# Kernel optimization log

Hardware: AMD Instinct MI355X
Metric: run time of the kernel (lower is better)

Reference implementation:

```python
import jax, jax.numpy as jnp
import numpy as np

B, S, H = 2, 1024, 2048
NH, HD = 16, 128
L = 4  # num_prev_layers == attention_window


def _rope(x):
    # x: [..., S, D]; standard rotate-half RoPE, base 10000
    d = x.shape[-1]
    s = x.shape[-2]
    inv_freq = 1.0 / (10000.0 ** (jnp.arange(0, d, 2, dtype=jnp.float32) / d))
    freqs = jnp.outer(jnp.arange(s, dtype=jnp.float32), inv_freq)  # [S, d/2]
    cos, sin = jnp.cos(freqs), jnp.sin(freqs)
    x1, x2 = jnp.split(x, 2, axis=-1)
    return jnp.concatenate([x1 * cos - x2 * sin, x2 * cos + x1 * sin], axis=-1)


def setup_inputs() -> dict:
    key = jax.random.key(0)
    ks = jax.random.split(key, 8)
    std = 0.02
    return {
        "hidden_states": jax.random.normal(ks[0], (B, S, H), jnp.float32),
        "prev_hidden_states": jax.random.normal(ks[1], (L, B, S, H), jnp.float32),
        "Wq": jax.random.normal(ks[2], (H, NH * HD), jnp.float32) * std,
        "bq": jnp.zeros((NH * HD,), jnp.float32),
        "Wk": jax.random.normal(ks[3], (H, NH * HD), jnp.float32) * std,
        "bk": jnp.zeros((NH * HD,), jnp.float32),
        "Wv": jax.random.normal(ks[4], (H, NH * HD), jnp.float32) * std,
        "bv": jnp.zeros((NH * HD,), jnp.float32),
        "Wo": jax.random.normal(ks[5], (NH * HD, H), jnp.float32) * std,
        "bo": jnp.zeros((H,), jnp.float32),
        "Wg": jax.random.normal(ks[6], (H, L), jnp.float32) * std,
    }


def reference(hidden_states, prev_hidden_states, Wq, bq, Wk, bk, Wv, bv, Wo, bo, Wg):
    b, s, _ = hidden_states.shape
    # queries from current layer: [b, nh, s, hd], RoPE applied
    q = (hidden_states @ Wq + bq).reshape(b, s, NH, HD).transpose(0, 2, 1, 3)
    q = _rope(q)
    # keys/values from each prev layer: [L, b, nh, s, hd]
    k = (prev_hidden_states @ Wk + bk).reshape(L, b, s, NH, HD).transpose(0, 1, 3, 2, 4)
    k = _rope(k)
    v = (prev_hidden_states @ Wv + bv).reshape(L, b, s, NH, HD).transpose(0, 1, 3, 2, 4)
    # per-prev-layer attention (no mask)
    scores = jnp.einsum('bhqd,lbhkd->lbhqk', q, k) / jnp.sqrt(jnp.float32(HD))
    attn = jax.nn.softmax(scores, axis=-1)
    lo = jnp.einsum('lbhqk,lbhkd->lbhqd', attn, v)
    lo = lo.transpose(0, 1, 3, 2, 4).reshape(L, b, s, NH * HD)  # merge heads
    # softmax gate over pooled queries -> combine layer outputs
    layer_w = jax.nn.softmax(jnp.mean(hidden_states, axis=1) @ Wg, axis=-1)  # [b, L]
    out = jnp.einsum('lbsh,bl->bsh', lo, layer_w)
    return out @ Wo + bo
```

## Files before the change

kernel.cpp:

```cpp
#include <hip/hip_runtime.h>
#include <hip/hip_bf16.h>
#include <math.h>


typedef __bf16 bf16;
typedef __bf16 bf16x4v __attribute__((ext_vector_type(4)));
typedef __bf16 bf16x8 __attribute__((ext_vector_type(8)));
typedef float f32x4 __attribute__((ext_vector_type(4)));

#define DEV static __device__ __forceinline__

DEV void gload_lds16(const void* g, void* s) {
  __builtin_amdgcn_global_load_lds(
      (const __attribute__((address_space(1))) void*)g,
      (__attribute__((address_space(3))) void*)s, 16, 0, 0);
}

DEV f32x4 mfma16(bf16x8 a, bf16x8 b, f32x4 c) {
  return __builtin_amdgcn_mfma_f32_16x16x32_bf16(a, b, c, 0, 0, 0);
}

__global__ __launch_bounds__(256) void cvt_kernel(const float* __restrict__ in,
                                                  bf16* __restrict__ out, int n4) {
  int i = blockIdx.x * 256 + threadIdx.x;
  if (i >= n4) return;
  const float4 v = ((const float4*)in)[i];
  bf16x4v o;
  o.x = (bf16)v.x; o.y = (bf16)v.y; o.z = (bf16)v.z; o.w = (bf16)v.w;
  ((bf16x4v*)out)[i] = o;
}

__global__ __launch_bounds__(256) void twt_kernel(const float* __restrict__ W,
                                                  bf16* __restrict__ Wt) {
  __shared__ float tile[64][65];
  const int t = threadIdx.x;
  const int n0 = blockIdx.x * 64, k0 = blockIdx.y * 64;
#pragma unroll
  for (int ph = 0; ph < 16; ++ph) {
    int idx = ph * 256 + t, r = idx >> 6, c = idx & 63;
    tile[r][c] = W[(size_t)(k0 + r) * 2048 + n0 + c];
  }
  __syncthreads();
#pragma unroll
  for (int ph = 0; ph < 16; ++ph) {
    int idx = ph * 256 + t, r = idx >> 6, c = idx & 63;
    Wt[(size_t)(n0 + r) * 2048 + k0 + c] = (bf16)tile[c][r];
  }
}

__global__ __launch_bounds__(64) void rope_table_kernel(float* __restrict__ cosT,
                                                        float* __restrict__ sinT) {
  int s = blockIdx.x, j = threadIdx.x;
  float inv = powf(10000.0f, -(float)j * (1.0f / 64.0f));
  float a = (float)s * inv;
  cosT[s * 64 + j] = cosf(a);
  sinT[s * 64 + j] = sinf(a);
}

__global__ __launch_bounds__(256) void rope_kernel(const bf16* __restrict__ raw,
                                                   const float* __restrict__ cosT,
                                                   const float* __restrict__ sinT,
                                                   bf16* __restrict__ outp) {
  int rid = blockIdx.x * 16 + (threadIdx.x >> 4);
  int j = threadIdx.x & 15;
  int s = rid & 1023;
  const bf16* src = raw + (size_t)rid * 128 + 4 * j;
  bf16* dst = outp + (size_t)rid * 128 + 4 * j;
  bf16x4v x1 = *(const bf16x4v*)src;
  bf16x4v x2 = *(const bf16x4v*)(src + 64);
  f32x4 c = *(const f32x4*)(cosT + s * 64 + 4 * j);
  f32x4 sn = *(const f32x4*)(sinT + s * 64 + 4 * j);
  bf16x4v o1, o2;
#pragma unroll
  for (int k = 0; k < 4; ++k) {
    float a = (float)x1[k], b2 = (float)x2[k];
    o1[k] = (bf16)(a * c[k] - b2 * sn[k]);
    o2[k] = (bf16)(b2 * c[k] + a * sn[k]);
  }
  *(bf16x4v*)dst = o1;
  *(bf16x4v*)(dst + 64) = o2;
}

__global__ __launch_bounds__(256) void mean_part_kernel(const float* __restrict__ hs,
                                                        float* __restrict__ part) {
  int bc = blockIdx.x;
  int b = bc >> 3, c0 = (bc & 7) * 256;
  int ss = blockIdx.y;
  int col = c0 + threadIdx.x;
  float s = 0.f;
  for (int r = 0; r < 128; ++r)
    s += hs[((size_t)b * 1024 + ss * 128 + r) * 2048 + col];
  part[(size_t)ss * 4096 + b * 2048 + col] = s;
}

__global__ __launch_bounds__(256) void mean_fin_kernel(const float* __restrict__ part,
                                                       float* __restrict__ meanb) {
  int c = blockIdx.x * 256 + threadIdx.x;
  float s = 0.f;
#pragma unroll
  for (int j = 0; j < 8; ++j) s += part[(size_t)j * 4096 + c];
  meanb[c] = s * (1.0f / 1024.0f);
}

__global__ __launch_bounds__(256) void gate_kernel(const float* __restrict__ meanb,
                                                   const float* __restrict__ Wg,
                                                   float* __restrict__ lwout) {
  __shared__ float red[8][256];
  int t = threadIdx.x;
  float p[8];
#pragma unroll
  for (int j = 0; j < 8; ++j) p[j] = 0.f;
  for (int hh = t; hh < 2048; hh += 256) {
    float m0 = meanb[hh], m1 = meanb[2048 + hh];
#pragma unroll
    for (int ll = 0; ll < 4; ++ll) {
      float g = Wg[hh * 4 + ll];
      p[ll] += m0 * g;
      p[4 + ll] += m1 * g;
    }
  }
#pragma unroll
  for (int j = 0; j < 8; ++j) red[j][t] = p[j];
  __syncthreads();
  for (int s2 = 128; s2 > 0; s2 >>= 1) {
    if (t < s2) {
#pragma unroll
      for (int j = 0; j < 8; ++j) red[j][t] += red[j][t + s2];
    }
    __syncthreads();
  }
  if (t == 0) {
#pragma unroll
    for (int bb = 0; bb < 2; ++bb) {
      float v0 = red[bb * 4 + 0][0], v1 = red[bb * 4 + 1][0];
      float v2 = red[bb * 4 + 2][0], v3 = red[bb * 4 + 3][0];
      float mx = fmaxf(fmaxf(v0, v1), fmaxf(v2, v3));
      float e0 = __expf(v0 - mx), e1 = __expf(v1 - mx);
      float e2 = __expf(v2 - mx), e3 = __expf(v3 - mx);
      float inv = 1.0f / (e0 + e1 + e2 + e3);
      lwout[bb * 4 + 0] = e0 * inv;
      lwout[bb * 4 + 1] = e1 * inv;
      lwout[bb * 4 + 2] = e2 * inv;
      lwout[bb * 4 + 3] = e3 * inv;
    }
  }
}

template <int OUTMODE>
__global__ __launch_bounds__(256) void gemm_kernel(const bf16* __restrict__ A,
                                                   const bf16* __restrict__ Bt,
                                                   const float* __restrict__ bias,
                                                   void* __restrict__ Cout,
                                                   int M, int N, int K) {
  __shared__ __attribute__((aligned(16))) bf16 As[2][128 * 64];
  __shared__ __attribute__((aligned(16))) bf16 Bs[2][128 * 64];
  const int t = threadIdx.x;
  const int w = t >> 6, l = t & 63;
  const int lo = l & 15, hi = l >> 4;
  const int wr = w >> 1, wc = w & 1;

  const int nwg = gridDim.x * gridDim.y;
  int flat = blockIdx.y * gridDim.x + blockIdx.x;
  int swz = (flat & 7) * (nwg >> 3) + (flat >> 3);
  const int bx = swz % gridDim.x, by = swz / gridDim.x;

  f32x4 acc[4][4];
#pragma unroll
  for (int m = 0; m < 4; ++m)
#pragma unroll
    for (int n = 0; n < 4; ++n)
#pragma unroll
      for (int q = 0; q < 4; ++q) acc[m][n][q] = 0.f;

  int srow[4], scl[4];
#pragma unroll
  for (int p = 0; p < 4; ++p) {
    int id = p * 256 + t;
    int r = id >> 3, cph = id & 7;
    srow[p] = r;
    scl[p] = cph ^ (r & 7);
  }

  const bf16* Ab = A + (size_t)by * 128 * K;
  const bf16* Bb = Bt + (size_t)bx * 128 * K;

  auto stage = [&](int bi, int kt) {
#pragma unroll
    for (int p = 0; p < 4; ++p)
      gload_lds16(Ab + (size_t)srow[p] * K + kt + scl[p] * 8,
                  &As[bi][(p * 256 + w * 64) * 8]);
#pragma unroll
    for (int p = 0; p < 4; ++p)
      gload_lds16(Bb + (size_t)srow[p] * K + kt + scl[p] * 8,
                  &Bs[bi][(p * 256 + w * 64) * 8]);
  };

  stage(0, 0);
  int cur = 0;
  for (int kt = 0; kt < K; kt += 64) {
    if (kt + 64 < K) {
      stage(cur ^ 1, kt + 64);
      asm volatile("s_waitcnt vmcnt(8)" ::: "memory");
    } else {
      asm volatile("s_waitcnt vmcnt(0)" ::: "memory");
    }
    __builtin_amdgcn_s_barrier();
    __builtin_amdgcn_sched_barrier(0);
    __builtin_amdgcn_s_setprio(1);
#pragma unroll
    for (int ks = 0; ks < 2; ++ks) {
      bf16x8 af[4], bfr[4];
#pragma unroll
      for (int m = 0; m < 4; ++m) {
        int row = wr * 64 + m * 16 + lo;
        int ch = (ks * 4 + hi) ^ (row & 7);
        af[m] = *(const bf16x8*)&As[cur][row * 64 + ch * 8];
      }
#pragma unroll
      for (int n = 0; n < 4; ++n) {
        int row = wc * 64 + n * 16 + lo;
        int ch = (ks * 4 + hi) ^ (row & 7);
        bfr[n] = *(const bf16x8*)&Bs[cur][row * 64 + ch * 8];
      }
#pragma unroll
      for (int m = 0; m < 4; ++m)
#pragma unroll
        for (int n = 0; n < 4; ++n)
          acc[m][n] = mfma16(af[m], bfr[n], acc[m][n]);
    }
    __builtin_amdgcn_s_setprio(0);
    __builtin_amdgcn_s_barrier();
    cur ^= 1;
  }

#pragma unroll
  for (int n = 0; n < 4; ++n) {
    int col = bx * 128 + wc * 64 + n * 16 + lo;
    float bb = bias[col];
#pragma unroll
    for (int m = 0; m < 4; ++m) {
#pragma unroll
      for (int i = 0; i < 4; ++i) {
        size_t row = (size_t)by * 128 + wr * 64 + m * 16 + hi * 4 + i;
        float v = acc[m][n][i] + bb;
        if (OUTMODE == 1)
          ((float*)Cout)[row * N + col] = v;
        else if (OUTMODE == 0)
          ((bf16*)Cout)[row * N + col] = (bf16)v;
        else {
          size_t g = (row >> 10) * 16 + (col >> 7);
          ((bf16*)Cout)[(g * 1024 + (row & 1023)) * 128 + (col & 127)] = (bf16)v;
        }
      }
    }
  }
}

__global__ __launch_bounds__(512, 2) void gemm_kv_kernel(
    const bf16* __restrict__ prev, const bf16* __restrict__ WkT,
    const bf16* __restrict__ WvT, const float* __restrict__ bk,
    const float* __restrict__ bv, const float* __restrict__ cosT,
    const float* __restrict__ sinT, bf16* __restrict__ Kout,
    bf16* __restrict__ Vout) {
  __shared__ __attribute__((aligned(16))) bf16 As[2][16384];
  __shared__ __attribute__((aligned(16))) bf16 Bs[2][16384];
  const int t = threadIdx.x;
  const int w = t >> 6, l = t & 63;
  const int lo = l & 15, hi = l >> 4;
  const int wm = w >> 2, wn = w & 3;

  const int bid = blockIdx.x;
  const int grp = bid >> 8;
  const int sub = bid & 255;
  const int swz = (sub & 7) * 32 + (sub >> 3);
  const int mt = (grp == 0) ? (swz >> 3) : (swz & 7);
  const int nt = (grp == 0) ? (swz & 7) : (swz >> 3);
  const bf16* Ab = ((grp == 0) ? prev : WvT) + (size_t)mt * 256 * 2048;
  const bf16* Bb = ((grp == 0) ? WkT : prev) + (size_t)nt * 256 * 2048;

  const int r0 = t >> 2;
  const int c8 = ((t & 3) ^ ((r0 >> 1) & 3)) * 8;
  int r0B = r0;
  if (grp == 0) {
    int a = r0 >> 5, rr = r0 & 31;
    r0B = (a == 0) ? rr : (a == 1) ? rr + 64 : (a == 2) ? rr + 32 : rr + 96;
  }

  f32x4 acc[8][4];
#pragma unroll
  for (int m = 0; m < 8; ++m)
#pragma unroll
    for (int n = 0; n < 4; ++n)
#pragma unroll
      for (int q = 0; q < 4; ++q) acc[m][n][q] = 0.f;

  auto gA = [&](int bi, int kh, int p, int koff) {
    gload_lds16(Ab + (size_t)(p * 128 + r0) * 2048 + koff + kh * 32 + c8,
                &As[bi][kh * 8192 + p * 4096 + w * 512]);
  };
  auto gB = [&](int bi, int kh, int p, int koff) {
    gload_lds16(Bb + (size_t)(p * 128 + r0B) * 2048 + koff + kh * 32 + c8,
                &Bs[bi][kh * 8192 + p * 4096 + w * 512]);
  };

  gA(0, 0, 0, 0); gA(0, 0, 1, 0);
  gB(0, 0, 0, 0); gB(0, 0, 1, 0);
  gA(0, 1, 0, 0); gA(0, 1, 1, 0);
  gB(0, 1, 0, 0); gB(0, 1, 1, 0);
  asm volatile("s_waitcnt vmcnt(4)" ::: "memory");
  __builtin_amdgcn_s_barrier();

  int cur = 0;
  for (int kt = 0; kt < 32; ++kt) {
    const int nxt = cur ^ 1;
    const int koff = (kt + 1) * 64;
    const bool pf = kt < 31;
    bf16x8 af[8], bfr[2];

#pragma unroll
    for (int m = 0; m < 8; ++m) {
      int row = wm * 128 + m * 16 + lo;
      int slot = hi ^ ((row >> 1) & 3);
      af[m] = *(const bf16x8*)&As[cur][row * 32 + slot * 8];
    }
#pragma unroll
    for (int n = 0; n < 2; ++n) {
      int row = wn * 64 + n * 16 + lo;
      int slot = hi ^ ((row >> 1) & 3);
      bfr[n] = *(const bf16x8*)&Bs[cur][row * 32 + slot * 8];
    }
    if (pf) { gA(nxt, 0, 0, koff); gA(nxt, 0, 1, koff); }
    __builtin_amdgcn_s_barrier();
    __builtin_amdgcn_s_setprio(1);
#pragma unroll
    for (int m = 0; m < 8; ++m) {
      acc[m][0] = mfma16(af[m], bfr[0], acc[m][0]);
      acc[m][1] = mfma16(af[m], bfr[1], acc[m][1]);
    }
    __builtin_amdgcn_s_setprio(0);
    __builtin_amdgcn_s_barrier();

#pragma unroll
    for (int n = 0; n < 2; ++n) {
      int row = wn * 64 + (n + 2) * 16 + lo;
      int slot = hi ^ ((row >> 1) & 3);
      bfr[n] = *(const bf16x8*)&Bs[cur][row * 32 + slot * 8];
    }
    if (pf) {
      gB(nxt, 0, 0, koff); gB(nxt, 0, 1, koff);
      asm volatile("s_waitcnt vmcnt(4)" ::: "memory");
    } else {
      asm volatile("s_waitcnt vmcnt(0)" ::: "memory");
    }
    __builtin_amdgcn_s_barrier();
    __builtin_amdgcn_s_setprio(1);
#pragma unroll
    for (int m = 0; m < 8; ++m) {
      acc[m][2] = mfma16(af[m], bfr[0], acc[m][2]);
      acc[m][3] = mfma16(af[m], bfr[1], acc[m][3]);
    }
    __builtin_amdgcn_s_setprio(0);
    __builtin_amdgcn_s_barrier();

#pragma unroll
    for (int m = 0; m < 8; ++m) {
      int row = wm * 128 + m * 16 + lo;
      int slot = hi ^ ((row >> 1) & 3);
      af[m] = *(const bf16x8*)&As[cur][8192 + row * 32 + slot * 8];
    }
#pragma unroll
    for (int n = 0; n < 2; ++n) {
      int row = wn * 64 + n * 16 + lo;
      int slot = hi ^ ((row >> 1) & 3);
      bfr[n] = *(const bf16x8*)&Bs[cur][8192 + row * 32 + slot * 8];
    }
    if (pf) { gA(nxt, 1, 0, koff); gA(nxt, 1, 1, koff); }
    __builtin_amdgcn_s_barrier();
    __builtin_amdgcn_s_setprio(1);
#pragma unroll
    for (int m = 0; m < 8; ++m) {
      acc[m][0] = mfma16(af[m], bfr[0], acc[m][0]);
      acc[m][1] = mfma16(af[m], bfr[1], acc[m][1]);
    }
    __builtin_amdgcn_s_setprio(0);
    __builtin_amdgcn_s_barrier();

#pragma unroll
    for (int n = 0; n < 2; ++n) {
      int row = wn * 64 + (n + 2) * 16 + lo;
      int slot = hi ^ ((row >> 1) & 3);
      bfr[n] = *(const bf16x8*)&Bs[cur][8192 + row * 32 + slot * 8];
    }
    if (pf) {
      gB(nxt, 1, 0, koff); gB(nxt, 1, 1, koff);
      asm volatile("s_waitcnt vmcnt(4)" ::: "memory");
    } else {
      asm volatile("s_waitcnt vmcnt(0)" ::: "memory");
    }
    __builtin_amdgcn_s_barrier();
    __builtin_amdgcn_s_setprio(1);
#pragma unroll
    for (int m = 0; m < 8; ++m) {
      acc[m][2] = mfma16(af[m], bfr[0], acc[m][2]);
      acc[m][3] = mfma16(af[m], bfr[1], acc[m][3]);
    }
    __builtin_amdgcn_s_setprio(0);
    __builtin_amdgcn_s_barrier();

    cur = nxt;
  }

  if (grp == 0) {
    const int headg = nt * 2 + (wn >> 1);
    const int jbase = (wn & 1) * 32;
#pragma unroll
    for (int n = 0; n < 2; ++n) {
      int j = jbase + n * 16 + lo;
      float bb1 = bk[headg * 128 + j];
      float bb2 = bk[headg * 128 + j + 64];
#pragma unroll
      for (int m = 0; m < 8; ++m) {
#pragma unroll
        for (int i = 0; i < 4; ++i) {
          size_t srow = (size_t)mt * 256 + wm * 128 + m * 16 + hi * 4 + i;
          int s_idx = (int)(srow & 1023);
          size_t g = (srow >> 10) * 16 + headg;
          float x1 = acc[m][n][i] + bb1;
          float x2 = acc[m][n + 2][i] + bb2;
          float cc = cosT[s_idx * 64 + j];
          float ss = sinT[s_idx * 64 + j];
          bf16* dst = Kout + (g * 1024 + s_idx) * 128;
          dst[j] = (bf16)(x1 * cc - x2 * ss);
          dst[j + 64] = (bf16)(x2 * cc + x1 * ss);
        }
      }
    }
  } else {
#pragma unroll
    for (int m = 0; m < 8; ++m) {
#pragma unroll
      for (int i = 0; i < 4; ++i) {
        size_t row = (size_t)mt * 256 + wm * 128 + m * 16 + hi * 4 + i;
        float rb = bv[row];
#pragma unroll
        for (int n = 0; n < 4; ++n) {
          int col = nt * 256 + wn * 64 + n * 16 + lo;
          int pos64 = ((n >> 1) << 5) + ((lo >> 2) << 3) + ((n & 1) << 2) + (lo & 3);
          int colp = (col & ~63) | pos64;
          float v = acc[m][n][i] + rb;
          Vout[(size_t)(colp >> 10) * 2097152 + row * 1024 + (colp & 1023)] =
              (bf16)v;
        }
      }
    }
  }
}

__global__ __launch_bounds__(256, 2) void attn_kernel(const bf16* __restrict__ Q,
                                                      const bf16* __restrict__ Kb,
                                                      const bf16* __restrict__ Vt,
                                                      const float* __restrict__ lw,
                                                      bf16* __restrict__ Obuf) {
  __shared__ __attribute__((aligned(16))) bf16 Ks[2][64 * 128];
  __shared__ __attribute__((aligned(16))) bf16 Vs[2][128 * 64];
  const int t = threadIdx.x, w = t >> 6, l = t & 63;
  const int lo = l & 15, hi = l >> 4;
  const int bh = blockIdx.x;
  const int qt = blockIdx.y;
  const int li = blockIdx.z;
  const int b = bh >> 4, h = bh & 15;
  const float C2 = 0.08838834764831845f * 1.44269504f;
  const float M2 = 64.0f * C2;

  bf16x8 qf[2][4];
#pragma unroll
  for (int qs = 0; qs < 2; ++qs) {
    const bf16* qptr =
        Q + ((size_t)bh * 1024 + qt * 128 + w * 32 + qs * 16 + lo) * 128;
#pragma unroll
    for (int db = 0; db < 4; ++db)
      qf[qs][db] = *(const bf16x8*)(qptr + db * 32 + hi * 8);
  }

  int krow[4], kcl[4], vrow[4], vcl[4];
#pragma unroll
  for (int p = 0; p < 4; ++p) {
    int id = p * 256 + t;
    krow[p] = id >> 4;
    kcl[p] = (id & 15) ^ (krow[p] & 7);
    vrow[p] = id >> 3;
    vcl[p] = (id & 7) ^ (vrow[p] & 7);
  }

  const bf16* Kl = Kb + ((size_t)li * 32 + bh) * (size_t)131072;
  const bf16* Vl = Vt + ((size_t)li * 32 + bh) * (size_t)131072;

  float si0 = 0.f, si1 = 0.f;
  f32x4 oacc[2][8];
#pragma unroll
  for (int qs = 0; qs < 2; ++qs)
#pragma unroll
    for (int dc = 0; dc < 8; ++dc)
#pragma unroll
      for (int q = 0; q < 4; ++q) oacc[qs][dc][q] = 0.f;

  auto stage = [&](int bi, int kt2) {
    const bf16* Ksrc = Kl + (size_t)kt2 * 8192;
#pragma unroll
    for (int p = 0; p < 4; ++p)
      gload_lds16(Ksrc + (size_t)krow[p] * 128 + kcl[p] * 8,
                  &Ks[bi][(p * 256 + w * 64) * 8]);
#pragma unroll
    for (int p = 0; p < 4; ++p)
      gload_lds16(Vl + (size_t)vrow[p] * 1024 + kt2 * 64 + vcl[p] * 8,
                  &Vs[bi][(p * 256 + w * 64) * 8]);
  };

  auto softmax_step = [&](f32x4 (&sa)[4], float& si, bf16x8 (&pf2)[2]) {
    float rs = 0.f;
    bf16x4v pk[4];
#pragma unroll
    for (int kc = 0; kc < 4; ++kc) {
#pragma unroll
      for (int i = 0; i < 4; ++i) {
        float pf_ = __builtin_amdgcn_exp2f(fmaf(sa[kc][i], C2, -M2));
        rs += pf_;
        pk[kc][i] = (bf16)pf_;
      }
    }
    rs += __shfl_xor(rs, 16);
    rs += __shfl_xor(rs, 32);
    si += rs;
    pf2[0] = __builtin_shufflevector(pk[0], pk[1], 0, 1, 2, 3, 4, 5, 6, 7);
    pf2[1] = __builtin_shufflevector(pk[2], pk[3], 0, 1, 2, 3, 4, 5, 6, 7);
  };

  stage(0, 0);
  int cur = 0;
  for (int kt = 0; kt < 16; ++kt) {
    if (kt < 15) {
      stage(cur ^ 1, kt + 1);
      asm volatile("s_waitcnt vmcnt(8)" ::: "memory");
    } else {
      asm volatile("s_waitcnt vmcnt(0)" ::: "memory");
    }
    __builtin_amdgcn_s_barrier();
    __builtin_amdgcn_sched_barrier(0);

    f32x4 sa[2][4];
#pragma unroll
    for (int qs = 0; qs < 2; ++qs)
#pragma unroll
      for (int kc = 0; kc < 4; ++kc)
#pragma unroll
        for (int q = 0; q < 4; ++q) sa[qs][kc][q] = 0.f;
    __builtin_amdgcn_s_setprio(1);
#pragma unroll
    for (int kc = 0; kc < 4; ++kc) {
      int row = kc * 16 + lo;
#pragma unroll
      for (int db = 0; db < 4; ++db) {
        int ch = (db * 4 + hi) ^ (row & 7);
        bf16x8 kf = *(const bf16x8*)&Ks[cur][row * 128 + ch * 8];
        sa[0][kc] = mfma16(kf, qf[0][db], sa[0][kc]);
        sa[1][kc] = mfma16(kf, qf[1][db], sa[1][kc]);
      }
    }
    __builtin_amdgcn_s_setprio(0);

    bf16x8 pfr[2][2];
    softmax_step(sa[0], si0, pfr[0]);
    softmax_step(sa[1], si1, pfr[1]);

    __builtin_amdgcn_s_setprio(1);
#pragma unroll
    for (int kvc = 0; kvc < 2; ++kvc) {
#pragma unroll
      for (int dc = 0; dc < 8; ++dc) {
        int rowv = dc * 16 + lo;
        int ch = (kvc * 4 + hi) ^ (rowv & 7);
        bf16x8 vf = *(const bf16x8*)&Vs[cur][rowv * 64 + ch * 8];
        oacc[0][dc] = mfma16(pfr[0][kvc], vf, oacc[0][dc]);
        oacc[1][dc] = mfma16(pfr[1][kvc], vf, oacc[1][dc]);
      }
    }
    __builtin_amdgcn_s_setprio(0);
    __builtin_amdgcn_s_barrier();
    cur ^= 1;
  }

  float wl = lw[b * 4 + li];
#pragma unroll
  for (int qs = 0; qs < 2; ++qs) {
    float sv = (qs == 0) ? si0 : si1;
    float inv[4];
#pragma unroll
    for (int i = 0; i < 4; ++i) inv[i] = wl / __shfl(sv, hi * 4 + i);
#pragma unroll
    for (int dc = 0; dc < 8; ++dc) {
      int col = h * 128 + dc * 16 + lo;
#pragma unroll
      for (int i = 0; i < 4; ++i) {
        int srow = qt * 128 + w * 32 + qs * 16 + hi * 4 + i;
        Obuf[((size_t)(li * 2 + b) * 1024 + srow) * 2048 + col] =
            (bf16)(oacc[qs][dc][i] * inv[i]);
      }
    }
  }
}

__global__ __launch_bounds__(256) void comb_kernel(const bf16* __restrict__ Obuf,
                                                   bf16* __restrict__ comb) {
  size_t i = ((size_t)blockIdx.x * 256 + threadIdx.x) * 8;
  bf16x8 a0 = *(const bf16x8*)(Obuf + i);
  bf16x8 a1 = *(const bf16x8*)(Obuf + 4194304 + i);
  bf16x8 a2 = *(const bf16x8*)(Obuf + 8388608 + i);
  bf16x8 a3 = *(const bf16x8*)(Obuf + 12582912 + i);
  bf16x8 o;
#pragma unroll
  for (int j = 0; j < 8; ++j)
    o[j] = (bf16)((float)a0[j] + (float)a1[j] + (float)a2[j] + (float)a3[j]);
  *(bf16x8*)(comb + i) = o;
}

extern "C" void kernel_launch(void* const* d_in, const int* in_sizes, int n_in,
                              void* d_out, int out_size, void* d_ws, size_t ws_size,
                              hipStream_t stream) {
  (void)in_sizes; (void)n_in; (void)out_size; (void)ws_size;
  const float* hs = (const float*)d_in[0];
  const float* prev = (const float*)d_in[1];
  const float* Wq = (const float*)d_in[2];
  const float* bq = (const float*)d_in[3];
  const float* Wk = (const float*)d_in[4];
  const float* bk = (const float*)d_in[5];
  const float* Wv = (const float*)d_in[6];
  const float* bv = (const float*)d_in[7];
  const float* Wo = (const float*)d_in[8];
  const float* bo = (const float*)d_in[9];
  const float* Wg = (const float*)d_in[10];
  float* out = (float*)d_out;

  char* ws = (char*)d_ws;
  bf16* hs_bf = (bf16*)(ws + 0);
  bf16* prev_bf = (bf16*)(ws + 8388608);
  bf16* WqT = (bf16*)(ws + 41943040);
  bf16* WkT = (bf16*)(ws + 50331648);
  bf16* WvT = (bf16*)(ws + 58720256);
  bf16* Qraw2 = (bf16*)(ws + 67108864);
  bf16* WoT = (bf16*)(ws + 75497472);
  bf16* Kbf = (bf16*)(ws + 83886080);
  bf16* Vt = (bf16*)(ws + 117440512);
  float* cosT = (float*)(ws + 150994944);
  float* sinT = (float*)(ws + 151257088);
  float* part = (float*)(ws + 151519232);
  float* meanb = (float*)(ws + 151650304);
  float* lwbuf = (float*)(ws + 151666688);
  bf16* Qbf = hs_bf;
  bf16* Obuf = prev_bf;
  bf16* comb = (bf16*)(ws + 0);

  cvt_kernel<<<4096, 256, 0, stream>>>(hs, hs_bf, 2048 * 2048 / 4);
  cvt_kernel<<<16384, 256, 0, stream>>>(prev, prev_bf, 8192 * 2048 / 4);

  twt_kernel<<<dim3(32, 32), 256, 0, stream>>>(Wq, WqT);
  twt_kernel<<<dim3(32, 32), 256, 0, stream>>>(Wk, WkT);
  twt_kernel<<<dim3(32, 32), 256, 0, stream>>>(Wv, WvT);
  twt_kernel<<<dim3(32, 32), 256, 0, stream>>>(Wo, WoT);

  rope_table_kernel<<<1024, 64, 0, stream>>>(cosT, sinT);
  mean_part_kernel<<<dim3(16, 8), 256, 0, stream>>>(hs, part);
  mean_fin_kernel<<<16, 256, 0, stream>>>(part, meanb);
  gate_kernel<<<1, 256, 0, stream>>>(meanb, Wg, lwbuf);

  gemm_kernel<3><<<dim3(16, 16), 256, 0, stream>>>(hs_bf, WqT, bq, Qraw2, 2048, 2048, 2048);
  gemm_kv_kernel<<<512, 512, 0, stream>>>(prev_bf, WkT, WvT, bk, bv, cosT, sinT,
                                          Kbf, Vt);

  rope_kernel<<<2048, 256, 0, stream>>>(Qraw2, cosT, sinT, Qbf);

  attn_kernel<<<dim3(32, 8, 4), 256, 0, stream>>>(Qbf, Kbf, Vt, lwbuf, Obuf);

  comb_kernel<<<2048, 256, 0, stream>>>(Obuf, comb);

  gemm_kernel<1><<<dim3(16, 16), 256, 0, stream>>>(comb, WoT, bo, out, 2048, 2048, 2048);
}
```

Baseline: 352.7 us.

## Fuse Q RoPE into GEMM epilogue, merge weight transposes, MFMA row sums

Q projection GEMM now permutes its B-tile rows so each wave holds both rotate-half partners, and applies bias plus RoPE directly in the epilogue. This removes the separate rope kernel and its extra pass over Q. The four weight transpose launches are merged into one 3D-grid launch. In attention, softmax row sums are computed with an MFMA against a ones vector instead of scalar adds and cross-lane shuffles, at the cost of extra MFMA work per tile.

Measured after the change: 338.3 us (median of 2 runs). -4.1%, faster.

```diff
diff --git a/kernel.cpp b/kernel.cpp
--- a/kernel.cpp
+++ b/kernel.cpp
@@ -30,8 +30,15 @@
   ((bf16x4v*)out)[i] = o;
 }
 
-__global__ __launch_bounds__(256) void twt_kernel(const float* __restrict__ W,
-                                                  bf16* __restrict__ Wt) {
+__global__ __launch_bounds__(256) void twt4_kernel(
+    const float* __restrict__ W0, const float* __restrict__ W1,
+    const float* __restrict__ W2, const float* __restrict__ W3,
+    bf16* __restrict__ T0, bf16* __restrict__ T1, bf16* __restrict__ T2,
+    bf16* __restrict__ T3) {
+  const float* W = (blockIdx.z == 0) ? W0 : (blockIdx.z == 1) ? W1
+                    : (blockIdx.z == 2) ? W2 : W3;
+  bf16* Wt = (blockIdx.z == 0) ? T0 : (blockIdx.z == 1) ? T1
+              : (blockIdx.z == 2) ? T2 : T3;
   __shared__ float tile[64][65];
   const int t = threadIdx.x;
   const int n0 = blockIdx.x * 64, k0 = blockIdx.y * 64;
@@ -55,30 +62,6 @@
   float a = (float)s * inv;
   cosT[s * 64 + j] = cosf(a);
   sinT[s * 64 + j] = sinf(a);
-}
-
-__global__ __launch_bounds__(256) void rope_kernel(const bf16* __restrict__ raw,
-                                                   const float* __restrict__ cosT,
-                                                   const float* __restrict__ sinT,
-                                                   bf16* __restrict__ outp) {
-  int rid = blockIdx.x * 16 + (threadIdx.x >> 4);
-  int j = threadIdx.x & 15;
-  int s = rid & 1023;
-  const bf16* src = raw + (size_t)rid * 128 + 4 * j;
-  bf16* dst = outp + (size_t)rid * 128 + 4 * j;
-  bf16x4v x1 = *(const bf16x4v*)src;
-  bf16x4v x2 = *(const bf16x4v*)(src + 64);
-  f32x4 c = *(const f32x4*)(cosT + s * 64 + 4 * j);
-  f32x4 sn = *(const f32x4*)(sinT + s * 64 + 4 * j);
-  bf16x4v o1, o2;
-#pragma unroll
-  for (int k = 0; k < 4; ++k) {
-    float a = (float)x1[k], b2 = (float)x2[k];
-    o1[k] = (bf16)(a * c[k] - b2 * sn[k]);
-    o2[k] = (bf16)(b2 * c[k] + a * sn[k]);
-  }
-  *(bf16x4v*)dst = o1;
-  *(bf16x4v*)(dst + 64) = o2;
 }
 
 __global__ __launch_bounds__(256) void mean_part_kernel(const float* __restrict__ hs,
@@ -151,7 +134,9 @@
                                                    const bf16* __restrict__ Bt,
                                                    const float* __restrict__ bias,
                                                    void* __restrict__ Cout,
-                                                   int M, int N, int K) {
+                                                   int M, int N, int K,
+                                                   const float* __restrict__ cosT,
+                                                   const float* __restrict__ sinT) {
   __shared__ __attribute__((aligned(16))) bf16 As[2][128 * 64];
   __shared__ __attribute__((aligned(16))) bf16 Bs[2][128 * 64];
   const int t = threadIdx.x;
@@ -172,13 +157,18 @@
 #pragma unroll
       for (int q = 0; q < 4; ++q) acc[m][n][q] = 0.f;
 
-  int srow[4], scl[4];
+  int srow[4], scl[4], srowB[4];
 #pragma unroll
   for (int p = 0; p < 4; ++p) {
     int id = p * 256 + t;
     int r = id >> 3, cph = id & 7;
     srow[p] = r;
     scl[p] = cph ^ (r & 7);
+    srowB[p] = r;
+    if (OUTMODE == 4) {
+      int a = r >> 5, rr = r & 31;
+      srowB[p] = (a == 0) ? rr : (a == 1) ? rr + 64 : (a == 2) ? rr + 32 : rr + 96;
+    }
   }
 
   const bf16* Ab = A + (size_t)by * 128 * K;
@@ -191,7 +181,7 @@
                   &As[bi][(p * 256 + w * 64) * 8]);
 #pragma unroll
     for (int p = 0; p < 4; ++p)
-      gload_lds16(Bb + (size_t)srow[p] * K + kt + scl[p] * 8,
+      gload_lds16(Bb + (size_t)srowB[p] * K + kt + scl[p] * 8,
                   &Bs[bi][(p * 256 + w * 64) * 8]);
   };
 
@@ -233,23 +223,42 @@
     cur ^= 1;
   }
 
-#pragma unroll
-  for (int n = 0; n < 4; ++n) {
-    int col = bx * 128 + wc * 64 + n * 16 + lo;
-    float bb = bias[col];
-#pragma unroll
-    for (int m = 0; m < 4; ++m) {
-#pragma unroll
-      for (int i = 0; i < 4; ++i) {
-        size_t row = (size_t)by * 128 + wr * 64 + m * 16 + hi * 4 + i;
-        float v = acc[m][n][i] + bb;
-        if (OUTMODE == 1)
+  if (OUTMODE == 4) {
+    const int jb = wc * 32;
+#pragma unroll
+    for (int n = 0; n < 2; ++n) {
+      int j = jb + n * 16 + lo;
+      float bb1 = bias[bx * 128 + j];
+      float bb2 = bias[bx * 128 + j + 64];
+#pragma unroll
+      for (int m = 0; m < 4; ++m) {
+#pragma unroll
+        for (int i = 0; i < 4; ++i) {
+          size_t row = (size_t)by * 128 + wr * 64 + m * 16 + hi * 4 + i;
+          int s_idx = (int)(row & 1023);
+          size_t g = (row >> 10) * 16 + bx;
+          float x1 = acc[m][n][i] + bb1;
+          float x2 = acc[m][n + 2][i] + bb2;
+          float cc = cosT[s_idx * 64 + j];
+          float ss = sinT[s_idx * 64 + j];
+          bf16* dst = (bf16*)Cout + (g * 1024 + s_idx) * 128;
+          dst[j] = (bf16)(x1 * cc - x2 * ss);
+          dst[j + 64] = (bf16)(x2 * cc + x1 * ss);
+        }
+      }
+    }
+  } else {
+#pragma unroll
+    for (int n = 0; n < 4; ++n) {
+      int col = bx * 128 + wc * 64 + n * 16 + lo;
+      float bb = bias[col];
+#pragma unroll
+      for (int m = 0; m < 4; ++m) {
+#pragma unroll
+        for (int i = 0; i < 4; ++i) {
+          size_t row = (size_t)by * 128 + wr * 64 + m * 16 + hi * 4 + i;
+          float v = acc[m][n][i] + bb;
           ((float*)Cout)[row * N + col] = v;
-        else if (OUTMODE == 0)
-          ((bf16*)Cout)[row * N + col] = (bf16)v;
-        else {
-          size_t g = (row >> 10) * 16 + (col >> 7);
-          ((bf16*)Cout)[(g * 1024 + (row & 1023)) * 128 + (col & 127)] = (bf16)v;
         }
       }
     }
@@ -471,6 +480,8 @@
   const int b = bh >> 4, h = bh & 15;
   const float C2 = 0.08838834764831845f * 1.44269504f;
   const float M2 = 64.0f * C2;
+  const bf16 one_ = (bf16)1.0f;
+  const bf16x8 ones8 = {one_, one_, one_, one_, one_, one_, one_, one_};
 
   bf16x8 qf[2][4];
 #pragma unroll
@@ -495,14 +506,17 @@
   const bf16* Kl = Kb + ((size_t)li * 32 + bh) * (size_t)131072;
   const bf16* Vl = Vt + ((size_t)li * 32 + bh) * (size_t)131072;
 
-  float si0 = 0.f, si1 = 0.f;
+  f32x4 dacc[2];
   f32x4 oacc[2][8];
 #pragma unroll
-  for (int qs = 0; qs < 2; ++qs)
+  for (int qs = 0; qs < 2; ++qs) {
+#pragma unroll
+    for (int q = 0; q < 4; ++q) dacc[qs][q] = 0.f;
 #pragma unroll
     for (int dc = 0; dc < 8; ++dc)
 #pragma unroll
       for (int q = 0; q < 4; ++q) oacc[qs][dc][q] = 0.f;
+  }
 
   auto stage = [&](int bi, int kt2) {
     const bf16* Ksrc = Kl + (size_t)kt2 * 8192;
@@ -516,21 +530,16 @@
                   &Vs[bi][(p * 256 + w * 64) * 8]);
   };
 
-  auto softmax_step = [&](f32x4 (&sa)[4], float& si, bf16x8 (&pf2)[2]) {
-    float rs = 0.f;
+  auto softmax_step = [&](f32x4 (&sa)[4], bf16x8 (&pf2)[2]) {
     bf16x4v pk[4];
 #pragma unroll
     for (int kc = 0; kc < 4; ++kc) {
 #pragma unroll
       for (int i = 0; i < 4; ++i) {
         float pf_ = __builtin_amdgcn_exp2f(fmaf(sa[kc][i], C2, -M2));
-        rs += pf_;
         pk[kc][i] = (bf16)pf_;
       }
     }
-    rs += __shfl_xor(rs, 16);
-    rs += __shfl_xor(rs, 32);
-    si += rs;
     pf2[0] = __builtin_shufflevector(pk[0], pk[1], 0, 1, 2, 3, 4, 5, 6, 7);
     pf2[1] = __builtin_shufflevector(pk[2], pk[3], 0, 1, 2, 3, 4, 5, 6, 7);
   };
@@ -569,12 +578,14 @@
     __builtin_amdgcn_s_setprio(0);
 
     bf16x8 pfr[2][2];
-    softmax_step(sa[0], si0, pfr[0]);
-    softmax_step(sa[1], si1, pfr[1]);
+    softmax_step(sa[0], pfr[0]);
+    softmax_step(sa[1], pfr[1]);
 
     __builtin_amdgcn_s_setprio(1);
 #pragma unroll
     for (int kvc = 0; kvc < 2; ++kvc) {
+      dacc[0] = mfma16(pfr[0][kvc], ones8, dacc[0]);
+      dacc[1] = mfma16(pfr[1][kvc], ones8, dacc[1]);
 #pragma unroll
       for (int dc = 0; dc < 8; ++dc) {
         int rowv = dc * 16 + lo;
@@ -592,10 +603,9 @@
   float wl = lw[b * 4 + li];
 #pragma unroll
   for (int qs = 0; qs < 2; ++qs) {
-    float sv = (qs == 0) ? si0 : si1;
     float inv[4];
 #pragma unroll
-    for (int i = 0; i < 4; ++i) inv[i] = wl / __shfl(sv, hi * 4 + i);
+    for (int i = 0; i < 4; ++i) inv[i] = wl / dacc[qs][i];
 #pragma unroll
     for (int dc = 0; dc < 8; ++dc) {
       int col = h * 128 + dc * 16 + lo;
@@ -646,7 +656,7 @@
   bf16* WqT = (bf16*)(ws + 41943040);
   bf16* WkT = (bf16*)(ws + 50331648);
   bf16* WvT = (bf16*)(ws + 58720256);
-  bf16* Qraw2 = (bf16*)(ws + 67108864);
+  bf16* Qbf = (bf16*)(ws + 67108864);
   bf16* WoT = (bf16*)(ws + 75497472);
   bf16* Kbf = (bf16*)(ws + 83886080);
   bf16* Vt = (bf16*)(ws + 117440512);
@@ -655,32 +665,29 @@
   float* part = (float*)(ws + 151519232);
   float* meanb = (float*)(ws + 151650304);
   float* lwbuf = (float*)(ws + 151666688);
-  bf16* Qbf = hs_bf;
   bf16* Obuf = prev_bf;
   bf16* comb = (bf16*)(ws + 0);
 
   cvt_kernel<<<4096, 256, 0, stream>>>(hs, hs_bf, 2048 * 2048 / 4);
   cvt_kernel<<<16384, 256, 0, stream>>>(prev, prev_bf, 8192 * 2048 / 4);
 
-  twt_kernel<<<dim3(32, 32), 256, 0, stream>>>(Wq, WqT);
-  twt_kernel<<<dim3(32, 32), 256, 0, stream>>>(Wk, WkT);
-  twt_kernel<<<dim3(32, 32), 256, 0, stream>>>(Wv, WvT);
-  twt_kernel<<<dim3(32, 32), 256, 0, stream>>>(Wo, WoT);
+  twt4_kernel<<<dim3(32, 32, 4), 256, 0, stream>>>(Wq, Wk, Wv, Wo, WqT, WkT,
+                                                   WvT, WoT);
 
   rope_table_kernel<<<1024, 64, 0, stream>>>(cosT, sinT);
   mean_part_kernel<<<dim3(16, 8), 256, 0, stream>>>(hs, part);
   mean_fin_kernel<<<16, 256, 0, stream>>>(part, meanb);
   gate_kernel<<<1, 256, 0, stream>>>(meanb, Wg, lwbuf);
 
-  gemm_kernel<3><<<dim3(16, 16), 256, 0, stream>>>(hs_bf, WqT, bq, Qraw2, 2048, 2048, 2048);
+  gemm_kernel<4><<<dim3(16, 16), 256, 0, stream>>>(hs_bf, WqT, bq, Qbf, 2048,
+                                                   2048, 2048, cosT, sinT);
   gemm_kv_kernel<<<512, 512, 0, stream>>>(prev_bf, WkT, WvT, bk, bv, cosT, sinT,
                                           Kbf, Vt);
 
-  rope_kernel<<<2048, 256, 0, stream>>>(Qraw2, cosT, sinT, Qbf);
-
   attn_kernel<<<dim3(32, 8, 4), 256, 0, stream>>>(Qbf, Kbf, Vt, lwbuf, Obuf);
 
   comb_kernel<<<2048, 256, 0, stream>>>(Obuf, comb);
 
-  gemm_kernel<1><<<dim3(16, 16), 256, 0, stream>>>(comb, WoT, bo, out, 2048, 2048, 2048);
-}
+  gemm_kernel<1><<<dim3(16, 16), 256, 0, stream>>>(comb, WoT, bo, out, 2048,
+                                                   2048, 2048, nullptr, nullptr);
+}
```
